# Kernel optimization log

Measured on AMD Instinct MI355X. Metric: run time of the kernel, lower is better.

The kernel has to match this reference:

```python
import jax, jax.numpy as jnp
import numpy as np

E = 1024
H = 8
D = E // H
WINDOW = 256
EPS = 1e-5


def layernorm(x, w, b):
    mu = jnp.mean(x, axis=-1, keepdims=True)
    var = jnp.mean((x - mu) ** 2, axis=-1, keepdims=True)
    return (x - mu) * jax.lax.rsqrt(var + EPS) * w + b


def setup_inputs() -> dict:
    key = jax.random.key(0)
    ks = jax.random.split(key, 12)
    B, T = 2, 2048
    s = 1.0 / np.sqrt(E)
    return {
        "x": jax.random.normal(ks[0], (B, T, E), jnp.float32),
        "ln1_w": jnp.ones((E,), jnp.float32),
        "ln1_b": jnp.zeros((E,), jnp.float32),
        "ln2_w": jnp.ones((E,), jnp.float32),
        "ln2_b": jnp.zeros((E,), jnp.float32),
        "in_proj_w": jax.random.normal(ks[1], (3 * E, E), jnp.float32) * s,
        "in_proj_b": jnp.zeros((3 * E,), jnp.float32),
        "out_w": jax.random.normal(ks[2], (E, E), jnp.float32) * s,
        "out_b": jnp.zeros((E,), jnp.float32),
        "w1": jax.random.normal(ks[3], (4 * E, E), jnp.float32) * s,
        "b1": jnp.zeros((4 * E,), jnp.float32),
        "w2": jax.random.normal(ks[4], (E, 4 * E), jnp.float32) * (1.0 / np.sqrt(4 * E)),
        "b2": jnp.zeros((E,), jnp.float32),
    }


def reference(x, ln1_w, ln1_b, ln2_w, ln2_b, in_proj_w, in_proj_b, out_w, out_b, w1, b1, w2, b2):
    B, T, _ = x.shape
    h = layernorm(x, ln1_w, ln1_b)
    # qkv projection: torch Linear is x @ W.T + b
    qkv = h @ in_proj_w.T + in_proj_b  # [B,T,3E]
    q, k, v = jnp.split(qkv, 3, axis=-1)
    q = q.reshape(B, T, H, D).transpose(0, 2, 1, 3)  # [B,H,T,D]
    k = k.reshape(B, T, H, D).transpose(0, 2, 1, 3)
    v = v.reshape(B, T, H, D).transpose(0, 2, 1, 3)
    scores = jnp.einsum("bhqd,bhkd->bhqk", q, k) / np.sqrt(D)
    idx = jnp.arange(T)
    row = idx[:, None]
    col = idx[None, :]
    # masked where future (col>row) OR outside window (col < row - WINDOW)
    allowed = (col <= row) & (col >= row - WINDOW)
    scores = jnp.where(allowed, scores, -jnp.inf)
    attn = jax.nn.softmax(scores, axis=-1)
    out = jnp.einsum("bhqk,bhkd->bhqd", attn, v)  # [B,H,T,D]
    out = out.transpose(0, 2, 1, 3).reshape(B, T, E)
    out = out @ out_w.T + out_b
    h2 = x + out
    m = layernorm(h2, ln2_w, ln2_b)
    m = jax.nn.relu(m @ w1.T + b1) @ w2.T + b2
    return h2 + m
```

## Files before the change

kernel.cpp:

```cpp
#include <hip/hip_runtime.h>

#define TOK 4096
#define EMB 1024

typedef __attribute__((ext_vector_type(8))) short s16x8;
typedef __attribute__((ext_vector_type(4))) float f32x4;

__device__ __forceinline__ unsigned short f2bf(float f) {
  union { float f; unsigned int u; } v; v.f = f;
  unsigned int r = v.u + 0x7FFFu + ((v.u >> 16) & 1u);
  return (unsigned short)(r >> 16);
}
__device__ __forceinline__ float bf2f(unsigned short u) {
  union { unsigned int u; float f; } v; v.u = ((unsigned int)u) << 16; return v.f;
}

#define GLOAD_LDS16(g, l) __builtin_amdgcn_global_load_lds( \
    (const __attribute__((address_space(1))) void*)(g), \
    (__attribute__((address_space(3))) void*)(l), 16, 0, 0)

template<int RELU, int PART, int NT>
__global__ __launch_bounds__(512)
void gemm256(const unsigned short* __restrict__ A,
             const unsigned short* __restrict__ B,
             const float* __restrict__ bias,
             unsigned short* __restrict__ C, int M, int N, int K)
{
  __shared__ unsigned short lds[2][2][128 * 128];
  const int tid = threadIdx.x;
  const int lane = tid & 63;
  const int w = tid >> 6;
  const int wr = w >> 2, wc = w & 3;
  const int l15 = lane & 15, lhi = lane >> 4;
  const int nbm = M >> 8;
  const int bm = blockIdx.x % nbm, bn = blockIdx.x / nbm;
  const int m0 = bm << 8, n0 = bn << 8;
  const int k0 = blockIdx.y * (NT * 64);

  const char* Abase = (const char*)(A + (size_t)m0 * K) + (size_t)k0 * 2;
  const char* Bbase = (const char*)(B + (size_t)n0 * K) + (size_t)k0 * 2;
  const size_t rowb = (size_t)K * 2;

  const int srt = tid >> 3;
  const int sccx = ((tid & 7) << 4) ^ ((srt & 7) << 4);
  const char* gA = Abase + (size_t)srt * rowb + sccx;
  const char* gB = Bbase + (size_t)srt * rowb + sccx;

  auto STAGE_A = [&](int ktl, int h, int p) {
    char* d = (char*)&lds[0][0][0] + p * 32768 + h * 16384 + (w << 10);
    const char* g = gA + (size_t)(h * 128) * rowb + ktl * 128;
    GLOAD_LDS16(g, d);
    GLOAD_LDS16(g + 64 * rowb, d + 8192);
  };
  auto STAGE_B = [&](int ktl, int h, int p) {
    char* d = (char*)&lds[1][0][0] + p * 32768 + h * 16384 + (w << 10);
    const char* g = gB + (size_t)(h * 128) * rowb + ktl * 128;
    GLOAD_LDS16(g, d);
    GLOAD_LDS16(g + 64 * rowb, d + 8192);
  };

  const int rdxor = (l15 & 7) << 4;
  const char* pA0 = (const char*)&lds[0][0][0] + (wr * 128 + l15) * 128 + ((0 * 64 + lhi * 16) ^ rdxor);
  const char* pA1 = (const char*)&lds[0][0][0] + (wr * 128 + l15) * 128 + ((1 * 64 + lhi * 16) ^ rdxor);
  const char* pB0 = (const char*)&lds[1][0][0] + (wc * 64 + l15) * 128 + ((0 * 64 + lhi * 16) ^ rdxor);
  const char* pB1 = (const char*)&lds[1][0][0] + (wc * 64 + l15) * 128 + ((1 * 64 + lhi * 16) ^ rdxor);

  f32x4 acc[8][4];
#pragma unroll
  for (int mf = 0; mf < 8; ++mf)
#pragma unroll
    for (int nf = 0; nf < 4; ++nf)
#pragma unroll
      for (int j = 0; j < 4; ++j) acc[mf][nf][j] = 0.f;

  STAGE_A(0, 0, 0); STAGE_A(0, 1, 0);
  STAGE_B(0, 0, 0); STAGE_B(0, 1, 0);
  STAGE_A(1, 0, 1); STAGE_A(1, 1, 1);
  STAGE_B(1, 0, 1);
  asm volatile("s_waitcnt vmcnt(6)" ::: "memory");
  __builtin_amdgcn_s_barrier();

  s16x8 af[8][2], bf[4][2];

#pragma unroll
  for (int kt = 0; kt < NT; ++kt) {
    const int P = (kt & 1) << 15;
    const int p = kt & 1;

#pragma unroll
    for (int mi = 0; mi < 4; ++mi) {
      af[mi][0] = *(const s16x8*)(pA0 + mi * 2048 + P);
      af[mi][1] = *(const s16x8*)(pA1 + mi * 2048 + P);
    }
#pragma unroll
    for (int ni = 0; ni < 2; ++ni) {
      bf[ni][0] = *(const s16x8*)(pB0 + ni * 2048 + P);
      bf[ni][1] = *(const s16x8*)(pB1 + ni * 2048 + P);
    }
#pragma unroll
    for (int mi = 4; mi < 8; ++mi) {
      af[mi][0] = *(const s16x8*)(pA0 + mi * 2048 + P);
      af[mi][1] = *(const s16x8*)(pA1 + mi * 2048 + P);
    }
#pragma unroll
    for (int ni = 2; ni < 4; ++ni) {
      bf[ni][0] = *(const s16x8*)(pB0 + ni * 2048 + P);
      bf[ni][1] = *(const s16x8*)(pB1 + ni * 2048 + P);
    }

    if (kt + 1 < NT) STAGE_B(kt + 1, 1, p ^ 1);

    __builtin_amdgcn_s_setprio(1);
#pragma unroll
    for (int mi = 0; mi < 4; ++mi)
#pragma unroll
      for (int ni = 0; ni < 2; ++ni)
#pragma unroll
        for (int ks = 0; ks < 2; ++ks)
          acc[mi][ni] = __builtin_amdgcn_mfma_f32_16x16x32_bf16(af[mi][ks], bf[ni][ks], acc[mi][ni], 0, 0, 0);
#pragma unroll
    for (int mi = 4; mi < 8; ++mi)
#pragma unroll
      for (int ni = 0; ni < 2; ++ni)
#pragma unroll
        for (int ks = 0; ks < 2; ++ks)
          acc[mi][ni] = __builtin_amdgcn_mfma_f32_16x16x32_bf16(af[mi][ks], bf[ni][ks], acc[mi][ni], 0, 0, 0);
#pragma unroll
    for (int mi = 0; mi < 4; ++mi)
#pragma unroll
      for (int ni = 2; ni < 4; ++ni)
#pragma unroll
        for (int ks = 0; ks < 2; ++ks)
          acc[mi][ni] = __builtin_amdgcn_mfma_f32_16x16x32_bf16(af[mi][ks], bf[ni][ks], acc[mi][ni], 0, 0, 0);
#pragma unroll
    for (int mi = 4; mi < 8; ++mi)
#pragma unroll
      for (int ni = 2; ni < 4; ++ni)
#pragma unroll
        for (int ks = 0; ks < 2; ++ks)
          acc[mi][ni] = __builtin_amdgcn_mfma_f32_16x16x32_bf16(af[mi][ks], bf[ni][ks], acc[mi][ni], 0, 0, 0);
    __builtin_amdgcn_s_setprio(0);

    __builtin_amdgcn_s_barrier();

    if (kt + 2 < NT) {
      STAGE_A(kt + 2, 0, p);
      STAGE_A(kt + 2, 1, p);
      STAGE_B(kt + 2, 0, p);
    }

    if (kt + 1 < NT) {
      if (kt + 2 < NT) asm volatile("s_waitcnt vmcnt(6)" ::: "memory");
      else             asm volatile("s_waitcnt vmcnt(0)" ::: "memory");
      __builtin_amdgcn_s_barrier();
    }
  }

  unsigned short* Cw = PART ? C + (size_t)blockIdx.y * M * N : C;
#pragma unroll
  for (int mf = 0; mf < 8; ++mf) {
    const int row = m0 + wr * 128 + mf * 16 + lhi * 4;
#pragma unroll
    for (int nf = 0; nf < 4; ++nf) {
      const int col = n0 + wc * 64 + nf * 16 + l15;
      const float bv = PART ? 0.f : bias[col];
#pragma unroll
      for (int j = 0; j < 4; ++j) {
        float v = acc[mf][nf][j] + bv;
        if (RELU) v = fmaxf(v, 0.f);
        Cw[(size_t)(row + j) * N + col] = f2bf(v);
      }
    }
  }
}

__global__ __launch_bounds__(256)
void reduce_add(const unsigned short* __restrict__ part, const unsigned short* __restrict__ res,
                const float* __restrict__ bias, float* __restrict__ out,
                int MN, int N, int S)
{
  const int i4 = (blockIdx.x * 256 + threadIdx.x) * 4;
  if (i4 >= MN) return;
  const int col = i4 & (N - 1);
  const ushort4 r = *(const ushort4*)(res + i4);
  float4 v;
  v.x = bf2f(r.x) + bias[col];
  v.y = bf2f(r.y) + bias[col + 1];
  v.z = bf2f(r.z) + bias[col + 2];
  v.w = bf2f(r.w) + bias[col + 3];
  for (int s = 0; s < S; ++s) {
    const ushort4 p = *(const ushort4*)(part + (size_t)s * MN + i4);
    v.x += bf2f(p.x); v.y += bf2f(p.y); v.z += bf2f(p.z); v.w += bf2f(p.w);
  }
  *(float4*)(out + i4) = v;
}

__global__ __launch_bounds__(256)
void reduce_ln(const unsigned short* __restrict__ part, const float* __restrict__ x,
               const float* __restrict__ ob, const float* __restrict__ ln_w,
               const float* __restrict__ ln_b, unsigned short* __restrict__ h2,
               unsigned short* __restrict__ m_in, int S)
{
  const int row = blockIdx.x;
  const int t = threadIdx.x;
  const size_t off = (size_t)row * EMB + t * 4;
  float4 v = *(const float4*)(x + off);
  const float4 obv = ((const float4*)ob)[t];
  v.x += obv.x; v.y += obv.y; v.z += obv.z; v.w += obv.w;
  for (int s = 0; s < S; ++s) {
    const ushort4 p = *(const ushort4*)(part + (size_t)s * TOK * EMB + off);
    v.x += bf2f(p.x); v.y += bf2f(p.y); v.z += bf2f(p.z); v.w += bf2f(p.w);
  }
  ushort4 hb;
  hb.x = f2bf(v.x); hb.y = f2bf(v.y); hb.z = f2bf(v.z); hb.w = f2bf(v.w);
  *(ushort4*)(h2 + off) = hb;

  float s1 = v.x + v.y + v.z + v.w;
  float sq = v.x * v.x + v.y * v.y + v.z * v.z + v.w * v.w;
#pragma unroll
  for (int o = 1; o < 64; o <<= 1) { s1 += __shfl_xor(s1, o); sq += __shfl_xor(sq, o); }
  __shared__ float red[8];
  if ((t & 63) == 0) { red[t >> 6] = s1; red[4 + (t >> 6)] = sq; }
  __syncthreads();
  s1 = red[0] + red[1] + red[2] + red[3];
  sq = red[4] + red[5] + red[6] + red[7];
  const float mu = s1 * (1.f / EMB);
  const float rs = rsqrtf(sq * (1.f / EMB) - mu * mu + 1e-5f);
  const float4 wv = ((const float4*)ln_w)[t];
  const float4 bv = ((const float4*)ln_b)[t];
  ushort4 o;
  o.x = f2bf((v.x - mu) * rs * wv.x + bv.x);
  o.y = f2bf((v.y - mu) * rs * wv.y + bv.y);
  o.z = f2bf((v.z - mu) * rs * wv.z + bv.z);
  o.w = f2bf((v.w - mu) * rs * wv.w + bv.w);
  ((ushort4*)(m_in + (size_t)row * EMB))[t] = o;
}

#define Q0 786432
#define Q1 (Q0 + 262144)
#define Q2 (Q1 + 1048576)
#define Q3 (Q2 + 1048576)
#define CVT_BLOCKS (Q3 / 256)
__global__ __launch_bounds__(256)
void prep(const float* __restrict__ w0, const float* __restrict__ w1s,
          const float* __restrict__ w2s, const float* __restrict__ w3s,
          unsigned short* __restrict__ d0, unsigned short* __restrict__ d1,
          unsigned short* __restrict__ d2, unsigned short* __restrict__ d3,
          const float* __restrict__ x, const float* __restrict__ ln_w,
          const float* __restrict__ ln_b, unsigned short* __restrict__ h)
{
  __shared__ float red[8];
  const int bid = blockIdx.x;
  const int t = threadIdx.x;
  if (bid < CVT_BLOCKS) {
    const int i = bid * 256 + t;
    const float* s; unsigned short* d; int off;
    if (i < Q0)      { s = w0;  d = d0; off = i; }
    else if (i < Q1) { s = w1s; d = d1; off = i - Q0; }
    else if (i < Q2) { s = w2s; d = d2; off = i - Q1; }
    else             { s = w3s; d = d3; off = i - Q2; }
    const float4 v = ((const float4*)s)[off];
    ushort4 o;
    o.x = f2bf(v.x); o.y = f2bf(v.y); o.z = f2bf(v.z); o.w = f2bf(v.w);
    ((ushort4*)d)[off] = o;
    return;
  }
  const int row = bid - CVT_BLOCKS;
  const float4 v = ((const float4*)(x + (size_t)row * EMB))[t];
  float sm = v.x + v.y + v.z + v.w;
  float sq = v.x * v.x + v.y * v.y + v.z * v.z + v.w * v.w;
#pragma unroll
  for (int off = 1; off < 64; off <<= 1) { sm += __shfl_xor(sm, off); sq += __shfl_xor(sq, off); }
  if ((t & 63) == 0) { red[t >> 6] = sm; red[4 + (t >> 6)] = sq; }
  __syncthreads();
  sm = red[0] + red[1] + red[2] + red[3];
  sq = red[4] + red[5] + red[6] + red[7];
  const float mu = sm * (1.f / EMB);
  const float rs = rsqrtf(sq * (1.f / EMB) - mu * mu + 1e-5f);
  const float4 wv = ((const float4*)ln_w)[t];
  const float4 bv = ((const float4*)ln_b)[t];
  ushort4 o;
  o.x = f2bf((v.x - mu) * rs * wv.x + bv.x);
  o.y = f2bf((v.y - mu) * rs * wv.y + bv.y);
  o.z = f2bf((v.z - mu) * rs * wv.z + bv.z);
  o.w = f2bf((v.w - mu) * rs * wv.w + bv.w);
  ((ushort4*)(h + (size_t)row * EMB))[t] = o;
}

__global__ __launch_bounds__(256)
void attn_win(const unsigned short* __restrict__ qkv, unsigned short* __restrict__ aout)
{
  __shared__ unsigned short Ks[64 * 136];
  __shared__ unsigned short Vt[128 * 72];
  __shared__ unsigned short Ps[4 * 16 * 72];
  const int bh = blockIdx.y;
  const int b = bh >> 3, hh = bh & 7;
  const int q0 = blockIdx.x << 6;
  const int tid = threadIdx.x, lane = tid & 63, w = tid >> 6;
  const int l15 = lane & 15, lhi = lane >> 4;
  const size_t base = (size_t)b * 2048 * 3072;

  s16x8 qf[4];
  {
    const unsigned short* qp = qkv + base + (size_t)(q0 + w * 16 + l15) * 3072 + hh * 128 + lhi * 8;
#pragma unroll
    for (int ks = 0; ks < 4; ++ks) qf[ks] = *(const s16x8*)(qp + ks * 32);
  }

  f32x4 o[8];
#pragma unroll
  for (int n = 0; n < 8; ++n)
#pragma unroll
    for (int j = 0; j < 4; ++j) o[n][j] = 0.f;
  float mrow[4] = {-1e30f, -1e30f, -1e30f, -1e30f};
  float lrow[4] = {0.f, 0.f, 0.f, 0.f};

  for (int t = 0; t < 5; ++t) {
    const int kt0 = q0 - 256 + t * 64;
    if (kt0 < 0) continue;
    __syncthreads();
    {
      const unsigned short* kg = qkv + base + (size_t)kt0 * 3072 + 1024 + hh * 128;
#pragma unroll
      for (int i = 0; i < 4; ++i) {
        const int c = tid + i * 256;
        const int r = c >> 4, cc = (c & 15) << 3;
        *(s16x8*)(Ks + r * 136 + cc) = *(const s16x8*)(kg + (size_t)r * 3072 + cc);
      }
      const unsigned short* vg = qkv + base + (size_t)kt0 * 3072 + 2048 + hh * 128;
#pragma unroll
      for (int i = 0; i < 2; ++i) {
        const int c = tid + i * 256;
        const int r2 = c >> 4, cc = (c & 15) << 3;
        s16x8 v0 = *(const s16x8*)(vg + (size_t)(2 * r2) * 3072 + cc);
        s16x8 v1 = *(const s16x8*)(vg + (size_t)(2 * r2 + 1) * 3072 + cc);
#pragma unroll
        for (int jj = 0; jj < 8; ++jj) {
          unsigned int pk = (unsigned int)(unsigned short)v0[jj] |
                            ((unsigned int)(unsigned short)v1[jj] << 16);
          *(unsigned int*)(Vt + (cc + jj) * 72 + 2 * r2) = pk;
        }
      }
    }
    __syncthreads();

    f32x4 s[4];
#pragma unroll
    for (int n = 0; n < 4; ++n)
#pragma unroll
      for (int j = 0; j < 4; ++j) s[n][j] = 0.f;
#pragma unroll
    for (int ks = 0; ks < 4; ++ks) {
#pragma unroll
      for (int n = 0; n < 4; ++n) {
        s16x8 kf = *(const s16x8*)(Ks + (n * 16 + l15) * 136 + ks * 32 + lhi * 8);
        s[n] = __builtin_amdgcn_mfma_f32_16x16x32_bf16(qf[ks], kf, s[n], 0, 0, 0);
      }
    }
    const bool mlo = (t == 0);
    const bool mhi = (kt0 == q0);
#pragma unroll
    for (int n = 0; n < 4; ++n) {
      const int kcol = n * 16 + l15;
#pragma unroll
      for (int j = 0; j < 4; ++j) {
        const int qrow = w * 16 + lhi * 4 + j;
        float v = s[n][j] * 0.08838834764831845f;
        if ((mlo && kcol < qrow) || (mhi && kcol > qrow)) v = -1e30f;
        s[n][j] = v;
      }
    }
    float alpha[4];
#pragma unroll
    for (int j = 0; j < 4; ++j) {
      float mx = fmaxf(fmaxf(s[0][j], s[1][j]), fmaxf(s[2][j], s[3][j]));
#pragma unroll
      for (int off = 1; off < 16; off <<= 1) mx = fmaxf(mx, __shfl_xor(mx, off));
      const float mn = fmaxf(mrow[j], mx);
      alpha[j] = __expf(mrow[j] - mn);
      mrow[j] = mn;
    }
    float rowsum[4] = {0.f, 0.f, 0.f, 0.f};
#pragma unroll
    for (int n = 0; n < 4; ++n)
#pragma unroll
      for (int j = 0; j < 4; ++j) {
        const float p = __expf(s[n][j] - mrow[j]);
        rowsum[j] += p;
        Ps[(w * 16 + lhi * 4 + j) * 72 + n * 16 + l15] = f2bf(p);
      }
#pragma unroll
    for (int j = 0; j < 4; ++j) {
      float rs = rowsum[j];
#pragma unroll
      for (int off = 1; off < 16; off <<= 1) rs += __shfl_xor(rs, off);
      lrow[j] = lrow[j] * alpha[j] + rs;
    }
#pragma unroll
    for (int n = 0; n < 8; ++n)
#pragma unroll
      for (int j = 0; j < 4; ++j) o[n][j] *= alpha[j];
#pragma unroll
    for (int ks = 0; ks < 2; ++ks) {
      const s16x8 pf = *(const s16x8*)(Ps + (w * 16 + l15) * 72 + ks * 32 + lhi * 8);
#pragma unroll
      for (int n = 0; n < 8; ++n) {
        const s16x8 vf = *(const s16x8*)(Vt + (n * 16 + l15) * 72 + ks * 32 + lhi * 8);
        o[n] = __builtin_amdgcn_mfma_f32_16x16x32_bf16(pf, vf, o[n], 0, 0, 0);
      }
    }
  }
  unsigned short* op = aout + (size_t)(b * 2048 + q0 + w * 16) * 1024 + hh * 128;
#pragma unroll
  for (int n = 0; n < 8; ++n)
#pragma unroll
    for (int j = 0; j < 4; ++j)
      op[(size_t)(lhi * 4 + j) * 1024 + n * 16 + l15] = f2bf(o[n][j] / lrow[j]);
}

extern "C" void kernel_launch(void* const* d_in, const int* in_sizes, int n_in,
                              void* d_out, int out_size, void* d_ws, size_t ws_size,
                              hipStream_t stream)
{
  (void)in_sizes; (void)n_in; (void)out_size; (void)ws_size;
  const float* x         = (const float*)d_in[0];
  const float* ln1_w     = (const float*)d_in[1];
  const float* ln1_b     = (const float*)d_in[2];
  const float* ln2_w     = (const float*)d_in[3];
  const float* ln2_b     = (const float*)d_in[4];
  const float* in_proj_w = (const float*)d_in[5];
  const float* in_proj_b = (const float*)d_in[6];
  const float* out_w     = (const float*)d_in[7];
  const float* out_b     = (const float*)d_in[8];
  const float* w1        = (const float*)d_in[9];
  const float* b1        = (const float*)d_in[10];
  const float* w2        = (const float*)d_in[11];
  const float* b2        = (const float*)d_in[12];
  float* out = (float*)d_out;

  char* ws = (char*)d_ws;
  unsigned short* h    = (unsigned short*)(ws);
  unsigned short* wqkv = (unsigned short*)(ws + (8u << 20));
  unsigned short* wout = (unsigned short*)(ws + (14u << 20));
  unsigned short* w1b  = (unsigned short*)(ws + (16u << 20));
  unsigned short* w2b  = (unsigned short*)(ws + (24u << 20));
  unsigned short* qkv  = (unsigned short*)(ws + (32u << 20));
  unsigned short* aout = (unsigned short*)(ws + (56u << 20));
  unsigned short* h2   = (unsigned short*)(ws + (64u << 20));
  unsigned short* m_in = (unsigned short*)(ws + (80u << 20));
  unsigned short* act  = (unsigned short*)(ws + (88u << 20));
  unsigned short* part_op = (unsigned short*)(ws + (88u << 20));
  unsigned short* part_m2 = (unsigned short*)(ws + (32u << 20));

  prep<<<dim3(CVT_BLOCKS + TOK), 256, 0, stream>>>(
      in_proj_w, out_w, w1, w2, wqkv, wout, w1b, w2b, x, ln1_w, ln1_b, h);

  gemm256<0, 0, 16><<<dim3(16 * 12), 512, 0, stream>>>(
      h, wqkv, in_proj_b, qkv, 4096, 3072, 1024);

  attn_win<<<dim3(32, 16), 256, 0, stream>>>(qkv, aout);

  gemm256<0, 1, 4><<<dim3(16 * 4, 4), 512, 0, stream>>>(
      aout, wout, nullptr, part_op, 4096, 1024, 1024);

  reduce_ln<<<dim3(TOK), 256, 0, stream>>>(part_op, x, out_b, ln2_w, ln2_b, h2, m_in, 4);

  gemm256<1, 0, 16><<<dim3(16 * 16), 512, 0, stream>>>(
      m_in, w1b, b1, act, 4096, 4096, 1024);

  gemm256<0, 1, 16><<<dim3(16 * 4, 4), 512, 0, stream>>>(
      act, w2b, nullptr, part_m2, 4096, 1024, 4096);

  reduce_add<<<dim3(4096 * 1024 / 4 / 256), 256, 0, stream>>>(
      part_m2, h2, b2, out, 4096 * 1024, 1024, 4);
}
```

Baseline: 187.4 us.

## Write transposed V from QKV GEMM epilogue and DMA it into attention LDS

The QKV GEMM epilogue now also writes a transposed copy of V (head dim by token) to a new workspace buffer. The attention kernel then loads V tiles straight into LDS with global_load_lds using an XOR-swizzled layout, replacing the per-thread register transpose and scalar LDS stores. It also raises wave priority around the MFMA loops. This adds an extra global write of V in the GEMM epilogue and a dependency on a larger workspace.

```diff
diff --git a/kernel.cpp b/kernel.cpp
--- a/kernel.cpp
+++ b/kernel.cpp
@@ -19,12 +19,13 @@
     (const __attribute__((address_space(1))) void*)(g), \
     (__attribute__((address_space(3))) void*)(l), 16, 0, 0)
 
-template<int RELU, int PART, int NT>
+template<int RELU, int PART, int NT, int VTR>
 __global__ __launch_bounds__(512)
 void gemm256(const unsigned short* __restrict__ A,
              const unsigned short* __restrict__ B,
              const float* __restrict__ bias,
-             unsigned short* __restrict__ C, int M, int N, int K)
+             unsigned short* __restrict__ C, int M, int N, int K,
+             unsigned short* __restrict__ vT)
 {
   __shared__ unsigned short lds[2][2][128 * 128];
   const int tid = threadIdx.x;
@@ -164,11 +165,18 @@
     for (int nf = 0; nf < 4; ++nf) {
       const int col = n0 + wc * 64 + nf * 16 + l15;
       const float bv = PART ? 0.f : bias[col];
+      ushort4 pk;
 #pragma unroll
       for (int j = 0; j < 4; ++j) {
         float v = acc[mf][nf][j] + bv;
         if (RELU) v = fmaxf(v, 0.f);
-        Cw[(size_t)(row + j) * N + col] = f2bf(v);
+        const unsigned short bb = f2bf(v);
+        Cw[(size_t)(row + j) * N + col] = bb;
+        if (VTR) { if (j == 0) pk.x = bb; else if (j == 1) pk.y = bb; else if (j == 2) pk.z = bb; else pk.w = bb; }
+      }
+      if (VTR && col >= 2048) {
+        const int dcol = col - 2048;
+        *(ushort4*)(vT + (size_t)dcol * 4096 + row) = pk;
       }
     }
   }
@@ -288,10 +296,11 @@
 }
 
 __global__ __launch_bounds__(256)
-void attn_win(const unsigned short* __restrict__ qkv, unsigned short* __restrict__ aout)
+void attn_win(const unsigned short* __restrict__ qkv, const unsigned short* __restrict__ vT,
+              unsigned short* __restrict__ aout)
 {
   __shared__ unsigned short Ks[64 * 136];
-  __shared__ unsigned short Vt[128 * 72];
+  __shared__ unsigned short Vt[128 * 64];
   __shared__ unsigned short Ps[4 * 16 * 72];
   const int bh = blockIdx.y;
   const int b = bh >> 3, hh = bh & 7;
@@ -307,6 +316,13 @@
     for (int ks = 0; ks < 4; ++ks) qf[ks] = *(const s16x8*)(qp + ks * 32);
   }
 
+  const int vrow = tid >> 3;
+  const int vcol = (((tid & 7) ^ ((tid >> 3) & 7)) << 4);
+  const char* vTbase = (const char*)(vT + (size_t)(hh * 128 + vrow) * 4096) + vcol;
+  char* vdst = (char*)&Vt[0] + (w << 10);
+  const char* pVrow = (const char*)&Vt[0] + l15 * 128;
+  const int vxor = (l15 & 7) << 4;
+
   f32x4 o[8];
 #pragma unroll
   for (int n = 0; n < 8; ++n)
@@ -327,20 +343,10 @@
         const int r = c >> 4, cc = (c & 15) << 3;
         *(s16x8*)(Ks + r * 136 + cc) = *(const s16x8*)(kg + (size_t)r * 3072 + cc);
       }
-      const unsigned short* vg = qkv + base + (size_t)kt0 * 3072 + 2048 + hh * 128;
-#pragma unroll
-      for (int i = 0; i < 2; ++i) {
-        const int c = tid + i * 256;
-        const int r2 = c >> 4, cc = (c & 15) << 3;
-        s16x8 v0 = *(const s16x8*)(vg + (size_t)(2 * r2) * 3072 + cc);
-        s16x8 v1 = *(const s16x8*)(vg + (size_t)(2 * r2 + 1) * 3072 + cc);
-#pragma unroll
-        for (int jj = 0; jj < 8; ++jj) {
-          unsigned int pk = (unsigned int)(unsigned short)v0[jj] |
-                            ((unsigned int)(unsigned short)v1[jj] << 16);
-          *(unsigned int*)(Vt + (cc + jj) * 72 + 2 * r2) = pk;
-        }
-      }
+      const char* vg = vTbase + (size_t)(b * 2048 + kt0) * 2;
+#pragma unroll
+      for (int c = 0; c < 4; ++c)
+        GLOAD_LDS16(vg + (size_t)(c * 32) * 8192, vdst + c * 4096);
     }
     __syncthreads();
 
@@ -349,6 +355,7 @@
     for (int n = 0; n < 4; ++n)
 #pragma unroll
       for (int j = 0; j < 4; ++j) s[n][j] = 0.f;
+    __builtin_amdgcn_s_setprio(1);
 #pragma unroll
     for (int ks = 0; ks < 4; ++ks) {
 #pragma unroll
@@ -357,6 +364,7 @@
         s[n] = __builtin_amdgcn_mfma_f32_16x16x32_bf16(qf[ks], kf, s[n], 0, 0, 0);
       }
     }
+    __builtin_amdgcn_s_setprio(0);
     const bool mlo = (t == 0);
     const bool mhi = (kt0 == q0);
 #pragma unroll
@@ -400,15 +408,18 @@
     for (int n = 0; n < 8; ++n)
 #pragma unroll
       for (int j = 0; j < 4; ++j) o[n][j] *= alpha[j];
+    __builtin_amdgcn_s_setprio(1);
 #pragma unroll
     for (int ks = 0; ks < 2; ++ks) {
       const s16x8 pf = *(const s16x8*)(Ps + (w * 16 + l15) * 72 + ks * 32 + lhi * 8);
+      const int cc = (ks * 64 + lhi * 16) ^ vxor;
 #pragma unroll
       for (int n = 0; n < 8; ++n) {
-        const s16x8 vf = *(const s16x8*)(Vt + (n * 16 + l15) * 72 + ks * 32 + lhi * 8);
+        const s16x8 vf = *(const s16x8*)(pVrow + n * 2048 + cc);
         o[n] = __builtin_amdgcn_mfma_f32_16x16x32_bf16(pf, vf, o[n], 0, 0, 0);
       }
     }
+    __builtin_amdgcn_s_setprio(0);
   }
   unsigned short* op = aout + (size_t)(b * 2048 + q0 + w * 16) * 1024 + hh * 128;
 #pragma unroll
@@ -451,25 +462,26 @@
   unsigned short* act  = (unsigned short*)(ws + (88u << 20));
   unsigned short* part_op = (unsigned short*)(ws + (88u << 20));
   unsigned short* part_m2 = (unsigned short*)(ws + (32u << 20));
+  unsigned short* vT   = (unsigned short*)(ws + (128u << 20));
 
   prep<<<dim3(CVT_BLOCKS + TOK), 256, 0, stream>>>(
       in_proj_w, out_w, w1, w2, wqkv, wout, w1b, w2b, x, ln1_w, ln1_b, h);
 
-  gemm256<0, 0, 16><<<dim3(16 * 12), 512, 0, stream>>>(
-      h, wqkv, in_proj_b, qkv, 4096, 3072, 1024);
-
-  attn_win<<<dim3(32, 16), 256, 0, stream>>>(qkv, aout);
-
-  gemm256<0, 1, 4><<<dim3(16 * 4, 4), 512, 0, stream>>>(
-      aout, wout, nullptr, part_op, 4096, 1024, 1024);
+  gemm256<0, 0, 16, 1><<<dim3(16 * 12), 512, 0, stream>>>(
+      h, wqkv, in_proj_b, qkv, 4096, 3072, 1024, vT);
+
+  attn_win<<<dim3(32, 16), 256, 0, stream>>>(qkv, vT, aout);
+
+  gemm256<0, 1, 4, 0><<<dim3(16 * 4, 4), 512, 0, stream>>>(
+      aout, wout, nullptr, part_op, 4096, 1024, 1024, nullptr);
 
   reduce_ln<<<dim3(TOK), 256, 0, stream>>>(part_op, x, out_b, ln2_w, ln2_b, h2, m_in, 4);
 
-  gemm256<1, 0, 16><<<dim3(16 * 16), 512, 0, stream>>>(
-      m_in, w1b, b1, act, 4096, 4096, 1024);
-
-  gemm256<0, 1, 16><<<dim3(16 * 4, 4), 512, 0, stream>>>(
-      act, w2b, nullptr, part_m2, 4096, 1024, 4096);
+  gemm256<1, 0, 16, 0><<<dim3(16 * 16), 512, 0, stream>>>(
+      m_in, w1b, b1, act, 4096, 4096, 1024, nullptr);
+
+  gemm256<0, 1, 16, 0><<<dim3(16 * 4, 4), 512, 0, stream>>>(
+      act, w2b, nullptr, part_m2, 4096, 1024, 4096, nullptr);
 
   reduce_add<<<dim3(4096 * 1024 / 4 / 256), 256, 0, stream>>>(
       part_m2, h2, b2, out, 4096 * 1024, 1024, 4);
```

Measured after the change: 187.9 us. About the same (+0.3%).
